# Optimization experiments

Measured on AMD Instinct MI355X. Metric: run time of the kernel, lower is better.

## Reference

```python
import jax, jax.numpy as jnp
import numpy as np

N_IMAGES = 2  # matches init kwarg


def setup_inputs() -> dict:
    key = jax.random.key(0)
    x = jax.random.normal(key, (8192, 128), dtype=jnp.float32)
    return {"x": x}


def reference(x):
    n_images = N_IMAGES
    N, D = x.shape
    P = N // n_images  # number of 'persons'
    G = x @ x.T  # [N, N] pairwise dot products (Gram matrix)

    # Offset pairs (i<j) within a window of n_images consecutive indices.
    # NB: original code uses range(person, person + n_images) -> sliding window.
    offs = np.array([(i, j) for i in range(n_images) for j in range(i + 1, n_images)])
    oi = jnp.asarray(offs[:, 0])  # [k]
    oj = jnp.asarray(offs[:, 1])  # [k]
    k = offs.shape[0]  # C(n_images, 2)

    p = jnp.arange(P)
    self_i = p[:, None] + oi[None, :]  # [P, k]
    self_j = p[:, None] + oj[None, :]  # [P, k]
    sim_self = jnp.min(G[self_i, self_j], axis=1)  # [P] min over self pairs

    # Upper-triangular (i<j) values; mask everything else to -inf.
    neg = jnp.finfo(G.dtype).min
    rows = jnp.arange(N)
    upper = jnp.where(rows[:, None] < rows[None, :], G, neg)

    # similarity_oth[p] = max over all i<j pairs excluding person p's k self pairs.
    # Only the global top-(k+1) values can ever be that max.
    top_vals, top_idx = jax.lax.top_k(upper.reshape(-1), k + 1)  # [k+1]
    self_flat = self_i * N + self_j  # [P, k] flat indices of self pairs
    member = (top_idx[None, :, None] == self_flat[:, None, :]).any(-1)  # [P, k+1]
    sim_oth = jnp.max(jnp.where(member, neg, top_vals[None, :]), axis=1)  # [P]

    return jnp.mean(sim_oth / sim_self)
```

## Files before the change

### kernel.cpp

```cpp
#include <hip/hip_runtime.h>
#include <hip/hip_bf16.h>
#include <math.h>
#include <float.h>

static constexpr int NN    = 8192;
static constexpr int DD    = 128;
static constexpr int PP    = 4096;
static constexpr int TILE  = 128;
static constexpr int TT    = NN / TILE;
static constexpr int NBLK  = TT * (TT + 1) / 2;
static constexpr int SSBLK = 64;
static constexpr int NC    = NBLK * 2;

struct Cand { float v; unsigned idx; };

using short8 = __attribute__((ext_vector_type(8))) short;
using f32x4  = __attribute__((ext_vector_type(4))) float;

__device__ __forceinline__ unsigned pk2(float lo, float hi) {
    unsigned a = (unsigned)__builtin_bit_cast(unsigned short, __float2bfloat16(lo));
    unsigned b = (unsigned)__builtin_bit_cast(unsigned short, __float2bfloat16(hi));
    return a | (b << 16);
}

__device__ __forceinline__ void push1(float& v1, unsigned& i1, float& v2, unsigned& i2,
                                      float w, unsigned j) {
    if (w > v1) { v2 = v1; i2 = i1; v1 = w; i1 = j; }
    else if (w > v2) { v2 = w; i2 = j; }
}

__device__ __forceinline__ void merge2(float& v1, unsigned& i1, float& v2, unsigned& i2,
                                       float w1, unsigned j1, float w2, unsigned j2) {
    if (w1 > v1) {
        float nv2; unsigned ni2;
        if (v1 >= w2) { nv2 = v1; ni2 = i1; } else { nv2 = w2; ni2 = j2; }
        v1 = w1; i1 = j1; v2 = nv2; i2 = ni2;
    } else if (w1 > v2) {
        v2 = w1; i2 = j1;
    }
}

__global__ __launch_bounds__(256) void k_top2(const float* __restrict__ x,
                                              Cand* __restrict__ cands,
                                              double* __restrict__ ss) {
    __shared__ uint4 As4[TILE * 16];
    __shared__ uint4 Bs4[TILE * 16];
    __shared__ float sv1[4], sv2[4];
    __shared__ unsigned si1[4], si2[4];

    const int tid  = threadIdx.x;
    const int wv   = tid >> 6;
    const int lane = tid & 63;

    if (blockIdx.x >= NBLK) {
        int b = blockIdx.x - NBLK;
        #pragma unroll 4
        for (int u = 0; u < 16; ++u) {
            int p = b * 64 + wv * 16 + u;
            const float* a  = x + (size_t)p * DD;
            const float* bb = a + DD;
            double s = (double)a[lane] * (double)bb[lane]
                     + (double)a[lane + 64] * (double)bb[lane + 64];
            #pragma unroll
            for (int off = 32; off >= 1; off >>= 1) s += __shfl_down(s, off);
            if (lane == 0) ss[p] = s;
        }
        return;
    }

    int rem = blockIdx.x;
    int ti = 0;
    while (rem >= TT - ti) { rem -= (TT - ti); ++ti; }
    int tj = ti + rem;

    #pragma unroll
    for (int it = 0; it < 8; ++it) {
        int g   = tid + 256 * it;
        int row = g >> 4;
        int c   = g & 15;
        int pos = row * 16 + (c ^ (row & 7));
        const float* sa = x + (size_t)(ti * TILE + row) * DD + c * 8;
        float4 a0 = *(const float4*)sa;
        float4 a1 = *(const float4*)(sa + 4);
        uint4 pa = {pk2(a0.x, a0.y), pk2(a0.z, a0.w), pk2(a1.x, a1.y), pk2(a1.z, a1.w)};
        As4[pos] = pa;
        const float* sb = x + (size_t)(tj * TILE + row) * DD + c * 8;
        float4 b0 = *(const float4*)sb;
        float4 b1 = *(const float4*)(sb + 4);
        uint4 pb = {pk2(b0.x, b0.y), pk2(b0.z, b0.w), pk2(b1.x, b1.y), pk2(b1.z, b1.w)};
        Bs4[pos] = pb;
    }
    __syncthreads();

    const int wm   = wv >> 1;
    const int wn   = wv & 1;
    const int quad = lane >> 4;
    const int r16  = lane & 15;
    const int swz  = r16 & 7;

    f32x4 acc[4][4];
    #pragma unroll
    for (int mi = 0; mi < 4; ++mi)
        #pragma unroll
        for (int nj = 0; nj < 4; ++nj)
            acc[mi][nj] = (f32x4){0.f, 0.f, 0.f, 0.f};

    #pragma unroll
    for (int s = 0; s < 4; ++s) {
        const int cc = (quad + 4 * s) ^ swz;
        short8 af[4], bfr[4];
        #pragma unroll
        for (int mi = 0; mi < 4; ++mi) {
            af[mi]  = __builtin_bit_cast(short8, As4[(wm * 64 + mi * 16 + r16) * 16 + cc]);
            bfr[mi] = __builtin_bit_cast(short8, Bs4[(wn * 64 + mi * 16 + r16) * 16 + cc]);
        }
        #pragma unroll
        for (int mi = 0; mi < 4; ++mi)
            #pragma unroll
            for (int nj = 0; nj < 4; ++nj)
                acc[mi][nj] = __builtin_amdgcn_mfma_f32_16x16x32_bf16(
                    af[mi], bfr[nj], acc[mi][nj], 0, 0, 0);
    }

    const int ibase = ti * TILE + wm * 64;
    const int jbase = tj * TILE + wn * 64;
    float v1 = -INFINITY, v2 = -INFINITY;
    unsigned i1 = 0, i2 = 0;
    #pragma unroll
    for (int mi = 0; mi < 4; ++mi) {
        #pragma unroll
        for (int nj = 0; nj < 4; ++nj) {
            int gj = jbase + nj * 16 + r16;
            #pragma unroll
            for (int reg = 0; reg < 4; ++reg) {
                int gi = ibase + mi * 16 + quad * 4 + reg;
                if (gi < gj) {
                    unsigned idx = (unsigned)(gi * NN + gj);
                    push1(v1, i1, v2, i2, acc[mi][nj][reg], idx);
                }
            }
        }
    }

    #pragma unroll
    for (int off = 32; off >= 1; off >>= 1) {
        float    w1 = __shfl_down(v1, off);
        unsigned j1 = (unsigned)__shfl_down((int)i1, off);
        float    w2 = __shfl_down(v2, off);
        unsigned j2 = (unsigned)__shfl_down((int)i2, off);
        merge2(v1, i1, v2, i2, w1, j1, w2, j2);
    }
    if (lane == 0) { sv1[wv] = v1; si1[wv] = i1; sv2[wv] = v2; si2[wv] = i2; }
    __syncthreads();
    if (tid == 0) {
        for (int w = 1; w < 4; ++w)
            merge2(v1, i1, v2, i2, sv1[w], si1[w], sv2[w], si2[w]);
        cands[blockIdx.x * 2]     = {v1, i1};
        cands[blockIdx.x * 2 + 1] = {v2, i2};
    }
}

__global__ __launch_bounds__(256) void k_final(const float* __restrict__ x,
                                               const double* __restrict__ ss,
                                               const Cand* __restrict__ cands,
                                               float* __restrict__ out) {
    __shared__ float redv[8];
    __shared__ float s_thresh;
    __shared__ int cnt;
    __shared__ unsigned qidx[128];
    __shared__ double qex[128];
    __shared__ double sd1, sd2;
    __shared__ unsigned stopi;
    __shared__ double sacc[256];

    const int tid  = threadIdx.x;
    const int wv   = tid >> 6;
    const int lane = tid & 63;
    if (tid == 0) cnt = 0;

    float v1 = -INFINITY, v2 = -INFINITY;
    for (int e = tid; e < NC; e += 256) {
        float v = cands[e].v;
        if (v > v1) { v2 = v1; v1 = v; }
        else if (v > v2) v2 = v;
    }
    #pragma unroll
    for (int off = 32; off >= 1; off >>= 1) {
        float w1 = __shfl_down(v1, off);
        float w2 = __shfl_down(v2, off);
        if (w1 > v1) { v2 = (v1 >= w2) ? v1 : w2; v1 = w1; }
        else if (w1 > v2) v2 = w1;
    }
    if (lane == 0) { redv[wv * 2] = v1; redv[wv * 2 + 1] = v2; }
    __syncthreads();
    if (tid == 0) {
        float a1 = -INFINITY, a2 = -INFINITY;
        for (int e = 0; e < 8; ++e) {
            float v = redv[e];
            if (v > a1) { a2 = a1; a1 = v; }
            else if (v > a2) a2 = v;
        }
        s_thresh = a2 - 1.0f;
    }
    __syncthreads();
    const float thresh = s_thresh;

    for (int e = tid; e < NC; e += 256) {
        if (cands[e].v >= thresh) {
            int k = atomicAdd(&cnt, 1);
            if (k < 128) qidx[k] = cands[e].idx;
        }
    }
    __syncthreads();
    const int n = cnt < 128 ? cnt : 128;

    for (int c = wv; c < n; c += 4) {
        unsigned idx = qidx[c];
        unsigned gi = idx >> 13;
        unsigned gj = idx & 8191;
        const float* pa = x + (size_t)gi * DD;
        const float* pb = x + (size_t)gj * DD;
        double s = (double)pa[lane] * (double)pb[lane]
                 + (double)pa[lane + 64] * (double)pb[lane + 64];
        #pragma unroll
        for (int off = 32; off >= 1; off >>= 1) s += __shfl_down(s, off);
        if (lane == 0) qex[c] = s;
    }
    __syncthreads();

    if (tid == 0) {
        double d1 = -DBL_MAX, d2 = -DBL_MAX;
        unsigned bi = 0;
        for (int c = 0; c < n; ++c) {
            double v = qex[c];
            if (v > d1) { d2 = d1; d1 = v; bi = qidx[c]; }
            else if (v > d2) d2 = v;
        }
        sd1 = d1; sd2 = d2; stopi = bi;
    }
    __syncthreads();

    const double top1 = sd1, top2 = sd2;
    const unsigned topi = stopi;

    double acc = 0.0;
    for (int p = tid; p < PP; p += 256) {
        unsigned selfidx = (unsigned)(p * NN + p + 1);
        double so = (topi == selfidx) ? top2 : top1;
        acc += so / ss[p];
    }
    sacc[tid] = acc;
    __syncthreads();
    for (int s = 128; s >= 1; s >>= 1) {
        if (tid < s) sacc[tid] += sacc[tid + s];
        __syncthreads();
    }
    if (tid == 0) out[0] = (float)(sacc[0] / (double)PP);
}

extern "C" void kernel_launch(void* const* d_in, const int* in_sizes, int n_in,
                              void* d_out, int out_size, void* d_ws, size_t ws_size,
                              hipStream_t stream) {
    (void)in_sizes; (void)n_in; (void)out_size; (void)ws_size;
    const float* x = (const float*)d_in[0];
    float* out = (float*)d_out;

    double* ss  = (double*)d_ws;
    Cand* cands = (Cand*)((char*)d_ws + PP * sizeof(double));

    k_top2<<<NBLK + SSBLK, 256, 0, stream>>>(x, cands, ss);
    k_final<<<1, 256, 0, stream>>>(x, ss, cands, out);
}
```

Measured before the change: 206.2 us.

## Pre-convert x to bf16 and stream tiles into LDS via direct DMA

Adds a prep kernel that converts x to bf16 once into workspace and also computes the self-pair dot products. The Gram tile kernel now loads bf16 tiles straight into padded LDS with global_load_lds, in two K-halves. This removes the repeated fp32 loads and in-kernel conversion done by every tile block, and halves LDS use so more blocks can be resident (launch bounds now ask for 4 per CU). The cost is an extra kernel launch, a 2 MB bf16 buffer in workspace, and an extra barrier between the K stages.

```diff
diff --git a/kernel.cpp b/kernel.cpp
--- a/kernel.cpp
+++ b/kernel.cpp
@@ -9,13 +9,23 @@
 static constexpr int TILE  = 128;
 static constexpr int TT    = NN / TILE;
 static constexpr int NBLK  = TT * (TT + 1) / 2;
-static constexpr int SSBLK = 64;
 static constexpr int NC    = NBLK * 2;
+static constexpr int GRP   = 1088;
+static constexpr int TLDS  = 16 * GRP;
 
 struct Cand { float v; unsigned idx; };
 
 using short8 = __attribute__((ext_vector_type(8))) short;
 using f32x4  = __attribute__((ext_vector_type(4))) float;
+
+typedef const __attribute__((address_space(1))) unsigned int* gas_uint;
+typedef __attribute__((address_space(3))) unsigned int* las_uint;
+
+__device__ __forceinline__ void dma16(const void* g, const void* l) {
+    __builtin_amdgcn_global_load_lds(
+        (gas_uint)(unsigned long long)g,
+        (las_uint)(unsigned)(unsigned long long)l, 16, 0, 0);
+}
 
 __device__ __forceinline__ unsigned pk2(float lo, float hi) {
     unsigned a = (unsigned)__builtin_bit_cast(unsigned short, __float2bfloat16(lo));
@@ -40,20 +50,21 @@
     }
 }
 
-__global__ __launch_bounds__(256) void k_top2(const float* __restrict__ x,
-                                              Cand* __restrict__ cands,
+__global__ __launch_bounds__(256) void k_prep(const float* __restrict__ x,
+                                              unsigned short* __restrict__ xb,
                                               double* __restrict__ ss) {
-    __shared__ uint4 As4[TILE * 16];
-    __shared__ uint4 Bs4[TILE * 16];
-    __shared__ float sv1[4], sv2[4];
-    __shared__ unsigned si1[4], si2[4];
-
-    const int tid  = threadIdx.x;
-    const int wv   = tid >> 6;
-    const int lane = tid & 63;
-
-    if (blockIdx.x >= NBLK) {
-        int b = blockIdx.x - NBLK;
+    const int tid = threadIdx.x;
+    if (blockIdx.x < 256) {
+        int chunk = blockIdx.x * 256 + tid;
+        const float4* s = (const float4*)(x + (size_t)chunk * 16);
+        float4 f0 = s[0], f1 = s[1], f2 = s[2], f3 = s[3];
+        uint4 o0 = {pk2(f0.x, f0.y), pk2(f0.z, f0.w), pk2(f1.x, f1.y), pk2(f1.z, f1.w)};
+        uint4 o1 = {pk2(f2.x, f2.y), pk2(f2.z, f2.w), pk2(f3.x, f3.y), pk2(f3.z, f3.w)};
+        uint4* d = (uint4*)(xb + (size_t)chunk * 16);
+        d[0] = o0; d[1] = o1;
+    } else {
+        int b = blockIdx.x - 256;
+        const int wv = tid >> 6, lane = tid & 63;
         #pragma unroll 4
         for (int u = 0; u < 16; ++u) {
             int p = b * 64 + wv * 16 + u;
@@ -65,38 +76,32 @@
             for (int off = 32; off >= 1; off >>= 1) s += __shfl_down(s, off);
             if (lane == 0) ss[p] = s;
         }
-        return;
-    }
+    }
+}
+
+__global__ __launch_bounds__(256, 4) void k_top2(const unsigned short* __restrict__ xb,
+                                                 Cand* __restrict__ cands) {
+    __shared__ __align__(16) char AsB[TLDS];
+    __shared__ __align__(16) char BsB[TLDS];
+    __shared__ float sv1[4], sv2[4];
+    __shared__ unsigned si1[4], si2[4];
+
+    const int tid  = threadIdx.x;
+    const int wv   = tid >> 6;
+    const int lane = tid & 63;
 
     int rem = blockIdx.x;
     int ti = 0;
     while (rem >= TT - ti) { rem -= (TT - ti); ++ti; }
     int tj = ti + rem;
 
-    #pragma unroll
-    for (int it = 0; it < 8; ++it) {
-        int g   = tid + 256 * it;
-        int row = g >> 4;
-        int c   = g & 15;
-        int pos = row * 16 + (c ^ (row & 7));
-        const float* sa = x + (size_t)(ti * TILE + row) * DD + c * 8;
-        float4 a0 = *(const float4*)sa;
-        float4 a1 = *(const float4*)(sa + 4);
-        uint4 pa = {pk2(a0.x, a0.y), pk2(a0.z, a0.w), pk2(a1.x, a1.y), pk2(a1.z, a1.w)};
-        As4[pos] = pa;
-        const float* sb = x + (size_t)(tj * TILE + row) * DD + c * 8;
-        float4 b0 = *(const float4*)sb;
-        float4 b1 = *(const float4*)(sb + 4);
-        uint4 pb = {pk2(b0.x, b0.y), pk2(b0.z, b0.w), pk2(b1.x, b1.y), pk2(b1.z, b1.w)};
-        Bs4[pos] = pb;
-    }
-    __syncthreads();
-
     const int wm   = wv >> 1;
     const int wn   = wv & 1;
     const int quad = lane >> 4;
     const int r16  = lane & 15;
-    const int swz  = r16 & 7;
+
+    const int grow = lane >> 3;
+    const int gcol = (lane & 7) * 8;
 
     f32x4 acc[4][4];
     #pragma unroll
@@ -106,20 +111,40 @@
             acc[mi][nj] = (f32x4){0.f, 0.f, 0.f, 0.f};
 
     #pragma unroll
-    for (int s = 0; s < 4; ++s) {
-        const int cc = (quad + 4 * s) ^ swz;
-        short8 af[4], bfr[4];
-        #pragma unroll
-        for (int mi = 0; mi < 4; ++mi) {
-            af[mi]  = __builtin_bit_cast(short8, As4[(wm * 64 + mi * 16 + r16) * 16 + cc]);
-            bfr[mi] = __builtin_bit_cast(short8, Bs4[(wn * 64 + mi * 16 + r16) * 16 + cc]);
-        }
-        #pragma unroll
-        for (int mi = 0; mi < 4; ++mi)
+    for (int p = 0; p < 2; ++p) {
+        const int kk = p * 64;
+        if (p) __syncthreads();
+
+        #pragma unroll
+        for (int t = 0; t < 4; ++t) {
+            int g = wv * 4 + t;
+            const unsigned short* ga =
+                xb + (size_t)(ti * TILE + g * 8 + grow) * DD + kk + gcol;
+            dma16(ga, AsB + g * GRP);
+            const unsigned short* gb =
+                xb + (size_t)(tj * TILE + g * 8 + grow) * DD + kk + gcol;
+            dma16(gb, BsB + g * GRP);
+        }
+        __syncthreads();
+
+        #pragma unroll
+        for (int s = 0; s < 2; ++s) {
+            const int cc = quad + 4 * s;
+            short8 af[4], bfr[4];
             #pragma unroll
-            for (int nj = 0; nj < 4; ++nj)
-                acc[mi][nj] = __builtin_amdgcn_mfma_f32_16x16x32_bf16(
-                    af[mi], bfr[nj], acc[mi][nj], 0, 0, 0);
+            for (int mi = 0; mi < 4; ++mi) {
+                int ra = wm * 64 + mi * 16 + r16;
+                af[mi] = *(const short8*)(AsB + (ra >> 3) * GRP + (ra & 7) * 128 + cc * 16);
+                int rb = wn * 64 + mi * 16 + r16;
+                bfr[mi] = *(const short8*)(BsB + (rb >> 3) * GRP + (rb & 7) * 128 + cc * 16);
+            }
+            #pragma unroll
+            for (int mi = 0; mi < 4; ++mi)
+                #pragma unroll
+                for (int nj = 0; nj < 4; ++nj)
+                    acc[mi][nj] = __builtin_amdgcn_mfma_f32_16x16x32_bf16(
+                        af[mi], bfr[nj], acc[mi][nj], 0, 0, 0);
+        }
     }
 
     const int ibase = ti * TILE + wm * 64;
@@ -267,7 +292,9 @@
 
     double* ss  = (double*)d_ws;
     Cand* cands = (Cand*)((char*)d_ws + PP * sizeof(double));
-
-    k_top2<<<NBLK + SSBLK, 256, 0, stream>>>(x, cands, ss);
+    unsigned short* xb = (unsigned short*)((char*)d_ws + 131072);
+
+    k_prep<<<320, 256, 0, stream>>>(x, xb, ss);
+    k_top2<<<NBLK, 256, 0, stream>>>(xb, cands);
     k_final<<<1, 256, 0, stream>>>(x, ss, cands, out);
 }
```

After: 174.9 us. -15.2%, faster.

## Pre-pack bf16 inputs in MFMA fragment layout and drop shared-memory staging

Applied to the files above, without the earlier changes.

Adds a prep kernel that converts x to bf16 once, stored in a layout where each lane's MFMA fragment is a contiguous 16-byte load, and moves the self-pair dot products into that kernel. The top-2 kernel then loads operands straight from global memory into registers, with no LDS staging or barrier. It double-buffers the A fragments and computes one 16x16 output tile at a time, keeping fewer accumulators live so occupancy can rise (launch bounds 256,4). The costs are an extra kernel launch, a global round trip for the packed data, and reliance on L2 for operand reuse across blocks.

```diff
diff --git a/kernel.cpp b/kernel.cpp
--- a/kernel.cpp
+++ b/kernel.cpp
@@ -3,14 +3,12 @@
 #include <math.h>
 #include <float.h>
 
-static constexpr int NN    = 8192;
-static constexpr int DD    = 128;
-static constexpr int PP    = 4096;
-static constexpr int TILE  = 128;
-static constexpr int TT    = NN / TILE;
-static constexpr int NBLK  = TT * (TT + 1) / 2;
-static constexpr int SSBLK = 64;
-static constexpr int NC    = NBLK * 2;
+static constexpr int NN   = 8192;
+static constexpr int DD   = 128;
+static constexpr int PP   = 4096;
+static constexpr int TT   = 64;
+static constexpr int NBLK = TT * (TT + 1) / 2;
+static constexpr int NC   = NBLK * 2;
 
 struct Cand { float v; unsigned idx; };
 
@@ -40,20 +38,23 @@
     }
 }
 
-__global__ __launch_bounds__(256) void k_top2(const float* __restrict__ x,
-                                              Cand* __restrict__ cands,
+__global__ __launch_bounds__(256) void k_prep(const float* __restrict__ x,
+                                              char* __restrict__ xq,
                                               double* __restrict__ ss) {
-    __shared__ uint4 As4[TILE * 16];
-    __shared__ uint4 Bs4[TILE * 16];
-    __shared__ float sv1[4], sv2[4];
-    __shared__ unsigned si1[4], si2[4];
-
-    const int tid  = threadIdx.x;
-    const int wv   = tid >> 6;
-    const int lane = tid & 63;
-
-    if (blockIdx.x >= NBLK) {
-        int b = blockIdx.x - NBLK;
+    const int tid = threadIdx.x;
+    if (blockIdx.x < 512) {
+        int gg   = blockIdx.x * 256 + tid;
+        int grp  = gg >> 8;
+        int c    = (gg >> 4) & 15;
+        int rloc = gg & 15;
+        int r    = grp * 16 + rloc;
+        const float4* s = (const float4*)(x + (size_t)r * DD + c * 8);
+        float4 f0 = s[0], f1 = s[1];
+        uint4 o = {pk2(f0.x, f0.y), pk2(f0.z, f0.w), pk2(f1.x, f1.y), pk2(f1.z, f1.w)};
+        *(uint4*)(xq + (size_t)gg * 16) = o;
+    } else {
+        int b = blockIdx.x - 512;
+        const int wv = tid >> 6, lane = tid & 63;
         #pragma unroll 4
         for (int u = 0; u < 16; ++u) {
             int p = b * 64 + wv * 16 + u;
@@ -65,81 +66,72 @@
             for (int off = 32; off >= 1; off >>= 1) s += __shfl_down(s, off);
             if (lane == 0) ss[p] = s;
         }
-        return;
-    }
+    }
+}
+
+__global__ __launch_bounds__(256, 4) void k_top2(const char* __restrict__ xq,
+                                                 Cand* __restrict__ cands) {
+    __shared__ float sv1[4], sv2[4];
+    __shared__ unsigned si1[4], si2[4];
 
     int rem = blockIdx.x;
     int ti = 0;
     while (rem >= TT - ti) { rem -= (TT - ti); ++ti; }
     int tj = ti + rem;
 
-    #pragma unroll
-    for (int it = 0; it < 8; ++it) {
-        int g   = tid + 256 * it;
-        int row = g >> 4;
-        int c   = g & 15;
-        int pos = row * 16 + (c ^ (row & 7));
-        const float* sa = x + (size_t)(ti * TILE + row) * DD + c * 8;
-        float4 a0 = *(const float4*)sa;
-        float4 a1 = *(const float4*)(sa + 4);
-        uint4 pa = {pk2(a0.x, a0.y), pk2(a0.z, a0.w), pk2(a1.x, a1.y), pk2(a1.z, a1.w)};
-        As4[pos] = pa;
-        const float* sb = x + (size_t)(tj * TILE + row) * DD + c * 8;
-        float4 b0 = *(const float4*)sb;
-        float4 b1 = *(const float4*)(sb + 4);
-        uint4 pb = {pk2(b0.x, b0.y), pk2(b0.z, b0.w), pk2(b1.x, b1.y), pk2(b1.z, b1.w)};
-        Bs4[pos] = pb;
-    }
-    __syncthreads();
-
+    const int tid  = threadIdx.x;
+    const int wv   = tid >> 6;
+    const int lane = tid & 63;
+    const int quad = lane >> 4;
+    const int r16  = lane & 15;
     const int wm   = wv >> 1;
     const int wn   = wv & 1;
-    const int quad = lane >> 4;
-    const int r16  = lane & 15;
-    const int swz  = r16 & 7;
-
-    f32x4 acc[4][4];
-    #pragma unroll
-    for (int mi = 0; mi < 4; ++mi)
-        #pragma unroll
-        for (int nj = 0; nj < 4; ++nj)
-            acc[mi][nj] = (f32x4){0.f, 0.f, 0.f, 0.f};
-
-    #pragma unroll
-    for (int s = 0; s < 4; ++s) {
-        const int cc = (quad + 4 * s) ^ swz;
-        short8 af[4], bfr[4];
-        #pragma unroll
-        for (int mi = 0; mi < 4; ++mi) {
-            af[mi]  = __builtin_bit_cast(short8, As4[(wm * 64 + mi * 16 + r16) * 16 + cc]);
-            bfr[mi] = __builtin_bit_cast(short8, Bs4[(wn * 64 + mi * 16 + r16) * 16 + cc]);
-        }
-        #pragma unroll
-        for (int mi = 0; mi < 4; ++mi)
-            #pragma unroll
-            for (int nj = 0; nj < 4; ++nj)
-                acc[mi][nj] = __builtin_amdgcn_mfma_f32_16x16x32_bf16(
-                    af[mi], bfr[nj], acc[mi][nj], 0, 0, 0);
-    }
-
-    const int ibase = ti * TILE + wm * 64;
-    const int jbase = tj * TILE + wn * 64;
+
+    const char* fb = xq + (size_t)lane * 16;
+    const int jg = tj * 8 + wn * 4;
+    const int ig = ti * 8 + wm * 4;
+
+    short8 bf[4][4];
+    #pragma unroll
+    for (int gn = 0; gn < 4; ++gn)
+        #pragma unroll
+        for (int s = 0; s < 4; ++s)
+            bf[gn][s] = *(const short8*)(fb + (size_t)(jg + gn) * 4096 + s * 1024);
+
     float v1 = -INFINITY, v2 = -INFINITY;
     unsigned i1 = 0, i2 = 0;
-    #pragma unroll
-    for (int mi = 0; mi < 4; ++mi) {
-        #pragma unroll
-        for (int nj = 0; nj < 4; ++nj) {
-            int gj = jbase + nj * 16 + r16;
+
+    short8 am[4], an[4];
+    #pragma unroll
+    for (int s = 0; s < 4; ++s)
+        am[s] = *(const short8*)(fb + (size_t)ig * 4096 + s * 1024);
+
+    #pragma unroll
+    for (int gm = 0; gm < 4; ++gm) {
+        if (gm < 3) {
+            #pragma unroll
+            for (int s = 0; s < 4; ++s)
+                an[s] = *(const short8*)(fb + (size_t)(ig + gm + 1) * 4096 + s * 1024);
+        }
+        #pragma unroll
+        for (int gn = 0; gn < 4; ++gn) {
+            f32x4 a = __builtin_amdgcn_mfma_f32_16x16x32_bf16(
+                am[0], bf[gn][0], (f32x4){0.f, 0.f, 0.f, 0.f}, 0, 0, 0);
+            #pragma unroll
+            for (int s = 1; s < 4; ++s)
+                a = __builtin_amdgcn_mfma_f32_16x16x32_bf16(
+                    am[s], bf[gn][s], a, 0, 0, 0);
+            int gj  = (jg + gn) * 16 + r16;
+            int gib = (ig + gm) * 16 + quad * 4;
             #pragma unroll
             for (int reg = 0; reg < 4; ++reg) {
-                int gi = ibase + mi * 16 + quad * 4 + reg;
-                if (gi < gj) {
-                    unsigned idx = (unsigned)(gi * NN + gj);
-                    push1(v1, i1, v2, i2, acc[mi][nj][reg], idx);
-                }
+                int gi = gib + reg;
+                if (gi < gj)
+                    push1(v1, i1, v2, i2, a[reg], (unsigned)(gi * NN + gj));
             }
         }
+        #pragma unroll
+        for (int s = 0; s < 4; ++s) am[s] = an[s];
     }
 
     #pragma unroll
@@ -266,8 +258,10 @@
     float* out = (float*)d_out;
 
     double* ss  = (double*)d_ws;
-    Cand* cands = (Cand*)((char*)d_ws + PP * sizeof(double));
-
-    k_top2<<<NBLK + SSBLK, 256, 0, stream>>>(x, cands, ss);
+    Cand* cands = (Cand*)((char*)d_ws + 32768);
+    char* xq    = (char*)d_ws + 131072;
+
+    k_prep<<<576, 256, 0, stream>>>(x, xq, ss);
+    k_top2<<<NBLK, 256, 0, stream>>>(xq, cands);
     k_final<<<1, 256, 0, stream>>>(x, ss, cands, out);
 }
```

New measurement: 176.7 us. 14.3% less time.
